# Optimization experiments

Hardware: AMD Instinct MI355X
Metric: run time of the kernel (lower is better)

Reference implementation:

```python
import jax, jax.numpy as jnp
import numpy as np
from math import sqrt

D_MODEL = 1024
N_HEADS = 16
FFN = 4096
B, N = 2, 2048
EPS = 1e-5


def _layernorm(x, g, b):
    mu = jnp.mean(x, -1, keepdims=True)
    var = jnp.mean((x - mu) ** 2, -1, keepdims=True)
    return (x - mu) * jax.lax.rsqrt(var + EPS) * g + b


def setup_inputs() -> dict:
    key = jax.random.key(0)
    ks = jax.random.split(key, 12)
    s = 1.0 / sqrt(D_MODEL)
    sf = 1.0 / sqrt(FFN)
    inp = {
        "tgt": jax.random.normal(ks[0], (B, N, D_MODEL), jnp.float32),
        # True = masked. Causal: query i may attend to keys j <= i.
        "tgt_mask": jnp.triu(jnp.ones((N, N), jnp.bool_), k=1),
        "tgt_key_pad_mask": jnp.zeros((B, N), jnp.bool_),
        "Wq": jax.random.uniform(ks[1], (D_MODEL, D_MODEL), jnp.float32, -s, s),
        "Wk": jax.random.uniform(ks[2], (D_MODEL, D_MODEL), jnp.float32, -s, s),
        "Wv": jax.random.uniform(ks[3], (D_MODEL, D_MODEL), jnp.float32, -s, s),
        "Wo": jax.random.uniform(ks[4], (D_MODEL, D_MODEL), jnp.float32, -s, s),
        "bo": jax.random.uniform(ks[5], (D_MODEL,), jnp.float32, -s, s),
        "W1": jax.random.uniform(ks[6], (FFN, D_MODEL), jnp.float32, -s, s),
        "b1": jax.random.uniform(ks[7], (FFN,), jnp.float32, -s, s),
        "W2": jax.random.uniform(ks[8], (D_MODEL, FFN), jnp.float32, -sf, sf),
        "b2": jax.random.uniform(ks[9], (D_MODEL,), jnp.float32, -sf, sf),
        "g1": jnp.ones((D_MODEL,), jnp.float32),
        "beta1": jnp.zeros((D_MODEL,), jnp.float32),
        "g2": jnp.ones((D_MODEL,), jnp.float32),
        "beta2": jnp.zeros((D_MODEL,), jnp.float32),
    }
    return inp


def _mha(x, tgt_mask, pad_mask, Wq, Wk, Wv, Wo, bo):
    b, n, d = x.shape
    dk = d // N_HEADS
    q = (x @ Wq.T).reshape(b, n, N_HEADS, dk).transpose(0, 2, 1, 3)  # bhnd
    k = (x @ Wk.T).reshape(b, n, N_HEADS, dk).transpose(0, 2, 1, 3)
    v = (x @ Wv.T).reshape(b, n, N_HEADS, dk).transpose(0, 2, 1, 3)
    scores = jnp.einsum("bhqd,bhkd->bhqk", q, k) / sqrt(dk)
    mask = tgt_mask[None, None, :, :] | pad_mask[:, None, None, :]
    scores = jnp.where(mask, -jnp.inf, scores)
    att = jax.nn.softmax(scores, axis=-1)
    out = jnp.einsum("bhqk,bhkd->bhqd", att, v).transpose(0, 2, 1, 3).reshape(b, n, d)
    return out @ Wo.T + bo


def reference(tgt, tgt_mask, tgt_key_pad_mask, Wq, Wk, Wv, Wo, bo,
              W1, b1, W2, b2, g1, beta1, g2, beta2):
    # PostNorm logic (pre_norm=False), dropout=0 (eval)
    h = _mha(tgt, tgt_mask, tgt_key_pad_mask, Wq, Wk, Wv, Wo, bo)
    x = _layernorm(tgt + h, g1, beta1)
    m = jax.nn.gelu(x @ W1.T + b1, approximate=True) @ W2.T + b2
    return _layernorm(x + m, g2, beta2)
```

## Files before the change

### kernel.cpp

```cpp
#include <hip/hip_runtime.h>


#define DEV __device__ __forceinline__

typedef __attribute__((ext_vector_type(4)))  float f32x4;
typedef __attribute__((ext_vector_type(16))) float f32x16;
typedef __attribute__((ext_vector_type(8)))  short s16x8;

static constexpr int Bb   = 2;
static constexpr int NN   = 2048;
static constexpr int DM   = 1024;
static constexpr int HH   = 16;
static constexpr int DK   = 64;
static constexpr int FF   = 4096;
static constexpr int ROWS = Bb * NN;

#define AS1(p) ((const __attribute__((address_space(1))) void*)(p))
#define AS3(p) ((__attribute__((address_space(3))) void*)(p))

DEV unsigned short f2bf(float f) {
  unsigned u = __float_as_uint(f);
  u += 0x7fff + ((u >> 16) & 1);
  return (unsigned short)(u >> 16);
}
DEV float fexp2(float x) {
  float r;
  asm("v_exp_f32 %0, %1" : "=v"(r) : "v"(x));
  return r;
}
DEV unsigned cvtpk(float lo, float hi) {
  unsigned r;
  asm("v_cvt_pk_bf16_f32 %0, %1, %2" : "=v"(r) : "v"(lo), "v"(hi));
  return r;
}

__global__ __launch_bounds__(256) void k_cast7(
    const float* __restrict__ tgt, const float* __restrict__ Wq,
    const float* __restrict__ Wk, const float* __restrict__ Wv,
    const float* __restrict__ Wo, const float* __restrict__ W1,
    const float* __restrict__ W2,
    ushort* __restrict__ xb, ushort* __restrict__ wqb,
    ushort* __restrict__ w1b, ushort* __restrict__ w2b) {
  const int i = blockIdx.x * 256 + threadIdx.x;
  constexpr int S0 = 1048576;
  constexpr int S1 = 262144;
  const float4* src;
  ushort* dstp;
  if (i < S0)               { src = (const float4*)tgt + i;            dstp = xb  + (size_t)i * 4; }
  else if (i < S0 + S1)     { src = (const float4*)Wq + (i - S0);      dstp = wqb + (size_t)(i - S0) * 4; }
  else if (i < S0 + 2 * S1) { src = (const float4*)Wk + (i - S0 - S1); dstp = wqb + (size_t)(i - S0) * 4; }
  else if (i < S0 + 3 * S1) { src = (const float4*)Wv + (i - S0 - 2 * S1); dstp = wqb + (size_t)(i - S0) * 4; }
  else if (i < S0 + 4 * S1) { src = (const float4*)Wo + (i - S0 - 3 * S1); dstp = wqb + (size_t)(i - S0) * 4; }
  else if (i < 3 * S0)      { src = (const float4*)W1 + (i - 2 * S0);  dstp = w1b + (size_t)(i - 2 * S0) * 4; }
  else                      { src = (const float4*)W2 + (i - 3 * S0);  dstp = w2b + (size_t)(i - 3 * S0) * 4; }
  float4 v = *src;
  ushort4 o;
  o.x = f2bf(v.x); o.y = f2bf(v.y); o.z = f2bf(v.z); o.w = f2bf(v.w);
  *reinterpret_cast<ushort4*>(dstp) = o;
}

template <int EPI, int BN, bool QKV, int SPLITK>
__global__ __launch_bounds__(256) void k_gemm(
    const ushort* __restrict__ A, const ushort* __restrict__ Bt,
    const float* __restrict__ bias, const float* __restrict__ resid,
    ushort* __restrict__ Cb, float* __restrict__ Cf,
    int K, int nbx) {
  __shared__ ushort As[3][128][32];
  __shared__ ushort Bs[3][BN][32];

  const int t = threadIdx.x;
  const int lane = t & 63, w = t >> 6;
  const int lr = lane & 15, lg = lane >> 4;
  const int lrow = lane >> 2, lc8 = (lane & 3) * 8;

  const int nwg = gridDim.x;
  const int bid = blockIdx.x;
  const int q8 = nwg >> 3, r8 = nwg & 7;
  const int xcd = bid & 7, lin = bid >> 3;
  int wg = (xcd < r8 ? xcd * (q8 + 1) : r8 * (q8 + 1) + (xcd - r8) * q8) + lin;
  int kc = 0;
  if constexpr (SPLITK == 2) { kc = wg & 1; wg >>= 1; }
  const int band = wg / (4 * nbx);
  const int inn  = wg % (4 * nbx);
  const int by = band * 4 + (inn & 3);
  const int bx = inn >> 2;

  const int bRow = by * 128;
  const int bCol = bx * BN;
  const int Kc = K / SPLITK;
  const int kofs = kc * Kc;
  const int nk = Kc / 32;

  constexpr int NW = BN / 32;
  const int wRow = (w >> 1) * 64, wCol = (w & 1) * (BN / 2);

  const f32x4 zero = {0.f, 0.f, 0.f, 0.f};
  f32x4 acc[4][NW];
#pragma unroll
  for (int m = 0; m < 4; ++m)
#pragma unroll
    for (int n = 0; n < NW; ++n) acc[m][n] = zero;

  auto stage = [&](int buf, int tile) {
    const int kb = kofs + tile * 32;
#pragma unroll
    for (int i = 0; i < 2; ++i) {
      int rr = w * 32 + i * 16;
      __builtin_amdgcn_global_load_lds(
          AS1(A + (size_t)(bRow + rr + lrow) * K + kb + lc8),
          AS3(&As[buf][rr][0]), 16, 0, 0);
    }
#pragma unroll
    for (int i = 0; i < BN / 64; ++i) {
      int rr = w * (BN / 4) + i * 16;
      __builtin_amdgcn_global_load_lds(
          AS1(Bt + (size_t)(bCol + rr + lrow) * K + kb + lc8),
          AS3(&Bs[buf][rr][0]), 16, 0, 0);
    }
  };

  stage(0, 0);
  stage(1, 1);
  for (int tt = 0; tt < nk; ++tt) {
    const int cur = tt % 3;
    if (tt + 2 < nk) {
      stage((tt + 2) % 3, tt + 2);
      if constexpr (BN == 128) asm volatile("s_waitcnt vmcnt(8)" ::: "memory");
      else                     asm volatile("s_waitcnt vmcnt(6)" ::: "memory");
    } else if (tt + 1 < nk) {
      if constexpr (BN == 128) asm volatile("s_waitcnt vmcnt(4)" ::: "memory");
      else                     asm volatile("s_waitcnt vmcnt(3)" ::: "memory");
    } else {
      asm volatile("s_waitcnt vmcnt(0)" ::: "memory");
    }
    __builtin_amdgcn_s_barrier();
    __builtin_amdgcn_sched_barrier(0);

    s16x8 af[4], bfr[NW];
#pragma unroll
    for (int m = 0; m < 4; ++m)
      af[m] = *reinterpret_cast<const s16x8*>(&As[cur][wRow + m * 16 + lr][lg * 8]);
#pragma unroll
    for (int n = 0; n < NW; ++n)
      bfr[n] = *reinterpret_cast<const s16x8*>(&Bs[cur][wCol + n * 16 + lr][lg * 8]);
#pragma unroll
    for (int m = 0; m < 4; ++m)
#pragma unroll
      for (int n = 0; n < NW; ++n)
        acc[m][n] = __builtin_amdgcn_mfma_f32_16x16x32_bf16(af[m], bfr[n], acc[m][n], 0, 0, 0);

    asm volatile("s_waitcnt lgkmcnt(0)" ::: "memory");
    __builtin_amdgcn_s_barrier();
    __builtin_amdgcn_sched_barrier(0);
  }

  ushort* CbOut = Cb;
  int colBase = bCol, Ncols = nbx * BN, third = 0;
  if (QKV) {
    third = bCol >> 10;
    CbOut = Cb + (size_t)third * ROWS * DM;
    colBase = bCol & 1023;
    Ncols = DM;
  }
#pragma unroll
  for (int m = 0; m < 4; ++m) {
    int gr = bRow + wRow + m * 16 + lg * 4;
#pragma unroll
    for (int n = 0; n < NW; ++n) {
      int gc = colBase + wCol + n * 16 + lr;
      float bv = (EPI == 1 || EPI == 2) ? bias[gc] : 0.0f;
#pragma unroll
      for (int r = 0; r < 4; ++r) {
        int nr = gr + r;
        float v = acc[m][n][r] + bv;
        if (EPI == 3) {
          Cf[((size_t)kc * ROWS + nr) * Ncols + gc] = v;
        } else if (EPI == 2) {
          size_t idx = (size_t)nr * Ncols + gc;
          Cf[idx] = v + resid[idx];
        } else if (EPI == 1) {
          size_t idx = (size_t)nr * Ncols + gc;
          float u = v + 0.044715f * v * v * v;
          float g = v / (1.0f + __expf(-1.5957691216057308f * u));
          CbOut[idx] = f2bf(g);
        } else {
          int gcs = gc;
          if (QKV && third == 1)
            gcs = (gc & ~63) | ((gc ^ ((nr & 7) << 3)) & 63);
          CbOut[(size_t)nr * Ncols + gcs] = f2bf(v);
        }
      }
    }
  }
}

__global__ __launch_bounds__(256) void k_vt(const ushort* __restrict__ V,
                                            ushort* __restrict__ vT) {
  __shared__ ushort Ls[64][72];
  const int t = threadIdx.x;
  const int n0 = blockIdx.x * 64;
  const int bh = blockIdx.y;
  const int b = bh >> 4, h = bh & 15;
  const int n = t >> 2;
#pragma unroll
  for (int half = 0; half < 2; ++half) {
    int c8 = ((t & 3) + half * 4) * 8;
    int4 v = *reinterpret_cast<const int4*>(
        V + ((size_t)(b * NN + n0 + n)) * DM + h * DK + c8);
    *reinterpret_cast<int4*>(&Ls[n][c8]) = v;
  }
  __syncthreads();
  const int d = t >> 2;
#pragma unroll
  for (int half = 0; half < 2; ++half) {
    int c = (t & 3) + half * 4;
    ushort tmp[8];
#pragma unroll
    for (int j = 0; j < 8; ++j) tmp[j] = Ls[c * 8 + j][d];
    size_t out = ((size_t)bh * DK + d) * NN + n0 + ((c ^ (d & 7)) * 8);
    *reinterpret_cast<int4*>(vT + out) = *reinterpret_cast<const int4*>(tmp);
  }
}

template <int WB, int RED>
__global__ __launch_bounds__(256) void k_ln(const float* __restrict__ in,
                                            const float* __restrict__ p0,
                                            const float* __restrict__ p1,
                                            const float* __restrict__ pb,
                                            const float* __restrict__ g,
                                            const float* __restrict__ bta,
                                            float* __restrict__ outf,
                                            ushort* __restrict__ outb) {
  const int row = blockIdx.x;
  const int t = threadIdx.x;
  float4 v = reinterpret_cast<const float4*>(in + (size_t)row * DM)[t];
  if (RED) {
    float4 a = reinterpret_cast<const float4*>(p0 + (size_t)row * DM)[t];
    float4 b = reinterpret_cast<const float4*>(p1 + (size_t)row * DM)[t];
    float4 c = reinterpret_cast<const float4*>(pb)[t];
    v.x += a.x + b.x + c.x;
    v.y += a.y + b.y + c.y;
    v.z += a.z + b.z + c.z;
    v.w += a.w + b.w + c.w;
  }
  float s1 = v.x + v.y + v.z + v.w;
  float s2 = v.x * v.x + v.y * v.y + v.z * v.z + v.w * v.w;
#pragma unroll
  for (int m = 32; m; m >>= 1) {
    s1 += __shfl_xor(s1, m, 64);
    s2 += __shfl_xor(s2, m, 64);
  }
  __shared__ float red[2][4];
  if ((t & 63) == 0) { red[0][t >> 6] = s1; red[1][t >> 6] = s2; }
  __syncthreads();
  s1 = red[0][0] + red[0][1] + red[0][2] + red[0][3];
  s2 = red[1][0] + red[1][1] + red[1][2] + red[1][3];
  const float mu = s1 * (1.0f / DM);
  const float var = s2 * (1.0f / DM) - mu * mu;
  const float rstd = rsqrtf(var + 1e-5f);
  float4 gv = reinterpret_cast<const float4*>(g)[t];
  float4 bv = reinterpret_cast<const float4*>(bta)[t];
  float4 o;
  o.x = (v.x - mu) * rstd * gv.x + bv.x;
  o.y = (v.y - mu) * rstd * gv.y + bv.y;
  o.z = (v.z - mu) * rstd * gv.z + bv.z;
  o.w = (v.w - mu) * rstd * gv.w + bv.w;
  reinterpret_cast<float4*>(outf + (size_t)row * DM)[t] = o;
  if (WB) {
    ushort4 ob;
    ob.x = f2bf(o.x); ob.y = f2bf(o.y); ob.z = f2bf(o.z); ob.w = f2bf(o.w);
    reinterpret_cast<ushort4*>(outb + (size_t)row * DM)[t] = ob;
  }
}

static __device__ const unsigned char SCHED40[40][2] = {
  {15,0},{15,1},{15,2},{15,3}, {14,0},{14,1},{14,2},{14,3},
  {13,0},{13,1},{13,2},{13,3}, {12,0},{12,1},{12,2},{12,3},
  {11,0},{11,1},{11,2}, {10,0},{10,1},{10,2},
  {9,0},{9,1},{9,2}, {8,0},{8,1},{8,2},
  {7,0},{7,1}, {6,0},{6,1}, {5,0},{5,1}, {4,0},{4,1},
  {3,0},{2,0},{1,0},{0,0}};

__global__ __launch_bounds__(256) void k_attn(const ushort* __restrict__ Q,
                                              const ushort* __restrict__ Kb,
                                              const ushort* __restrict__ vT,
                                              ushort* __restrict__ O,
                                              float* __restrict__ Op,
                                              float* __restrict__ ml) {
  __shared__ ushort Ks[2][64 * 64];
  __shared__ ushort Vs[2][64 * 64];

  const int t = threadIdx.x;
  const int bid = blockIdx.x;
  const int xcd = bid & 7, j = bid >> 3;
  const int head = j & 3, e = j >> 2;
  const int qi = SCHED40[e][0], seg = SCHED40[e][1];
  const int bh = xcd * 4 + head;
  const int ntiles = 2 * qi + 2;
  const int nseg = (2 * qi + 9) >> 3;
  const int tb = ntiles / nseg, rem = ntiles % nseg;
  const int kt0 = seg * tb + (seg < rem ? seg : rem);
  const int kt1 = kt0 + tb + (seg < rem ? 1 : 0);

  const int lane = t & 63, wid = t >> 6;
  const int l31 = lane & 31, hi = lane >> 5;
  const int q0w = qi * 128 + wid * 32;
  const size_t qbase = ((size_t)(bh >> 4) * NN) * DM + (bh & 15) * DK;
  const size_t vbase = (size_t)bh * DK * NN;

  const float C = 0.18033688011112043f;

  s16x8 qf[4];
#pragma unroll
  for (int c = 0; c < 4; ++c)
    qf[c] = *reinterpret_cast<const s16x8*>(Q + qbase + (size_t)(q0w + l31) * DM + c * 16 + hi * 8);

  float mrun = -1e30f, lrun = 0.f, negcm = 1e30f;
  f32x16 accO[2];
#pragma unroll
  for (int dt = 0; dt < 2; ++dt)
#pragma unroll
    for (int r = 0; r < 16; ++r) accO[dt][r] = 0.f;

  auto stage = [&](int buf, int kt) {
    const int kk = kt * 64;
#pragma unroll
    for (int i = 0; i < 2; ++i) {
      int row0 = wid * 16 + i * 8;
      __builtin_amdgcn_global_load_lds(
          AS1(Kb + qbase + (size_t)(kk + row0 + (lane >> 3)) * DM + (lane & 7) * 8),
          AS3(&Ks[buf][row0 * 64]), 16, 0, 0);
      __builtin_amdgcn_global_load_lds(
          AS1(vT + vbase + (size_t)(row0 + (lane >> 3)) * NN + kk + (lane & 7) * 8),
          AS3(&Vs[buf][row0 * 64]), 16, 0, 0);
    }
  };

  stage(0, kt0);
  for (int kt = kt0, li = 0; kt < kt1; ++kt, ++li) {
    const int cur = li & 1;
    const int kk = kt * 64;
    __syncthreads();
    if (kt + 1 < kt1) stage(cur ^ 1, kt + 1);

    if (kk <= q0w + 31) {
      const char* KsB = (const char*)Ks[cur];
      const char* VsB = (const char*)Vs[cur];
      const bool diag = (kk + 64 > q0w);
      const int nsub = (kk + 32 <= q0w + 31) ? 2 : 1;

      f32x16 st[2];
      __builtin_amdgcn_s_setprio(1);
#pragma unroll
      for (int sub = 0; sub < 2; ++sub) {
        if (sub >= nsub) break;
#pragma unroll
        for (int r = 0; r < 16; ++r) st[sub][r] = 0.f;
        const int row = sub * 32 + l31;
        const int swz = (row & 7) << 4;
#pragma unroll
        for (int c = 0; c < 4; ++c) {
          s16x8 kf = *reinterpret_cast<const s16x8*>(KsB + row * 128 + ((c * 32 + hi * 16) ^ swz));
          st[sub] = __builtin_amdgcn_mfma_f32_32x32x16_bf16(kf, qf[c], st[sub], 0, 0, 0);
        }
      }
      __builtin_amdgcn_s_setprio(0);

      const int q = q0w + l31;
      float p[32];
#pragma unroll
      for (int sub = 0; sub < 2; ++sub) {
        if (sub >= nsub) break;
#pragma unroll
        for (int r = 0; r < 16; ++r) {
          float v = st[sub][r];
          if (diag) {
            int kl = sub * 32 + (r & 3) + 8 * (r >> 2) + 4 * hi;
            if (kk + kl > q) v = -1e30f;
          }
          p[sub * 16 + r] = v;
        }
      }
      float a[16];
#pragma unroll
      for (int i = 0; i < 16; ++i) a[i] = (nsub == 2) ? fmaxf(p[i], p[i + 16]) : p[i];
#pragma unroll
      for (int s = 8; s; s >>= 1)
#pragma unroll
        for (int i = 0; i < 8; ++i) if (i < s) a[i] = fmaxf(a[i], a[i + s]);
      float rm = fmaxf(a[0], __shfl_xor(a[0], 32, 64));

      if (__any(rm > mrun)) {
        const float mn = fmaxf(mrun, rm);
        const float alpha = fexp2(C * (mrun - mn));
        mrun = mn;
        negcm = -C * mn;
        lrun *= alpha;
#pragma unroll
        for (int dt = 0; dt < 2; ++dt) accO[dt] *= alpha;
      }

#pragma unroll
      for (int sub = 0; sub < 2; ++sub) {
        if (sub >= nsub) break;
#pragma unroll
        for (int i = 0; i < 16; ++i)
          p[sub * 16 + i] = fexp2(fmaf(p[sub * 16 + i], C, negcm));
      }
#pragma unroll
      for (int i = 0; i < 16; ++i) a[i] = (nsub == 2) ? (p[i] + p[i + 16]) : p[i];
#pragma unroll
      for (int s = 8; s; s >>= 1)
#pragma unroll
        for (int i = 0; i < 8; ++i) if (i < s) a[i] += a[i + s];
      lrun += a[0] + __shfl_xor(a[0], 32, 64);

      s16x8 pf[4];
#pragma unroll
      for (int sub = 0; sub < 2; ++sub) {
        if (sub >= nsub) break;
#pragma unroll
        for (int hf = 0; hf < 2; ++hf) {
          const float* pp = &p[sub * 16 + hf * 8];
          unsigned X0 = cvtpk(pp[0], pp[1]);
          unsigned X1 = cvtpk(pp[2], pp[3]);
          unsigned Y0 = cvtpk(pp[4], pp[5]);
          unsigned Y1 = cvtpk(pp[6], pp[7]);
          asm volatile("v_permlane32_swap_b32 %0, %1" : "+v"(X0), "+v"(Y0));
          asm volatile("v_permlane32_swap_b32 %0, %1" : "+v"(X1), "+v"(Y1));
          union { unsigned u[4]; s16x8 v; } uu;
          uu.u[0] = X0; uu.u[1] = X1; uu.u[2] = Y0; uu.u[3] = Y1;
          pf[sub * 2 + hf] = uu.v;
        }
      }

      __builtin_amdgcn_s_setprio(1);
#pragma unroll
      for (int dt = 0; dt < 2; ++dt) {
        const int d = dt * 32 + l31;
        const int vswz = (d & 7) << 4;
#pragma unroll
        for (int kc = 0; kc < 4; ++kc) {
          if (kc >= nsub * 2) break;
          s16x8 vf = *reinterpret_cast<const s16x8*>(VsB + d * 128 + ((kc * 32 + hi * 16) ^ vswz));
          accO[dt] = __builtin_amdgcn_mfma_f32_32x32x16_bf16(vf, pf[kc], accO[dt], 0, 0, 0);
        }
      }
      __builtin_amdgcn_s_setprio(0);
    }
  }

  if (nseg == 1) {
    const int q = q0w + l31;
    const float inv = 1.0f / lrun;
#pragma unroll
    for (int dt = 0; dt < 2; ++dt)
#pragma unroll
      for (int rg = 0; rg < 4; ++rg) {
        int d0 = 8 * rg + 4 * hi + 32 * dt;
        ushort4 ov;
        ov.x = f2bf(accO[dt][rg * 4 + 0] * inv);
        ov.y = f2bf(accO[dt][rg * 4 + 1] * inv);
        ov.z = f2bf(accO[dt][rg * 4 + 2] * inv);
        ov.w = f2bf(accO[dt][rg * 4 + 3] * inv);
        *reinterpret_cast<ushort4*>(O + qbase + (size_t)q * DM + d0) = ov;
      }
  } else {
    const int pidx = (bh * 12 + (qi - 4)) * 4 + seg;
    float* op = Op + (size_t)pidx * (128 * 64);
    const int row = wid * 32 + l31;
#pragma unroll
    for (int dt = 0; dt < 2; ++dt)
#pragma unroll
      for (int rg = 0; rg < 4; ++rg) {
        int d0 = 8 * rg + 4 * hi + 32 * dt;
        f32x4 v4 = { accO[dt][rg * 4 + 0], accO[dt][rg * 4 + 1],
                     accO[dt][rg * 4 + 2], accO[dt][rg * 4 + 3] };
        *reinterpret_cast<f32x4*>(op + (size_t)row * 64 + d0) = v4;
      }
    if (hi == 0) {
      ml[(size_t)pidx * 256 + row * 2 + 0] = mrun;
      ml[(size_t)pidx * 256 + row * 2 + 1] = lrun;
    }
  }
}

__global__ __launch_bounds__(256) void k_amerge(const float* __restrict__ Op,
                                                const float* __restrict__ ml,
                                                ushort* __restrict__ O) {
  const int bid = blockIdx.x;
  const int bh = bid / 12, qq = bid % 12;
  const int qi = qq + 4;
  const int nseg = (2 * qi + 9) >> 3;
  const int t = threadIdx.x;
  const int row = t >> 1, dh = (t & 1) * 32;
  const float C = 0.18033688011112043f;
  const int pbase = (bh * 12 + qq) * 4;

  float M = -1e30f;
  for (int s = 0; s < nseg; ++s)
    M = fmaxf(M, ml[(size_t)(pbase + s) * 256 + row * 2 + 0]);
  float wsum = 0.f;
  for (int s = 0; s < nseg; ++s) {
    float ms = ml[(size_t)(pbase + s) * 256 + row * 2 + 0];
    float ls = ml[(size_t)(pbase + s) * 256 + row * 2 + 1];
    wsum += ls * fexp2(C * (ms - M));
  }
  const float inv = 1.0f / wsum;

  f32x4 acc[8];
#pragma unroll
  for (int i = 0; i < 8; ++i) acc[i] = (f32x4){0.f, 0.f, 0.f, 0.f};
  for (int s = 0; s < nseg; ++s) {
    float ws = fexp2(C * (ml[(size_t)(pbase + s) * 256 + row * 2 + 0] - M));
    const float* os = Op + (size_t)(pbase + s) * (128 * 64) + (size_t)row * 64 + dh;
#pragma unroll
    for (int i = 0; i < 8; ++i) {
      f32x4 v = reinterpret_cast<const f32x4*>(os)[i];
      acc[i] += v * ws;
    }
  }

  const int b = bh >> 4, h = bh & 15;
  const int n = qi * 128 + row;
  ushort* dst = O + ((size_t)(b * NN + n)) * DM + h * DK + dh;
#pragma unroll
  for (int i = 0; i < 8; ++i) {
    ushort4 ov;
    ov.x = f2bf(acc[i][0] * inv);
    ov.y = f2bf(acc[i][1] * inv);
    ov.z = f2bf(acc[i][2] * inv);
    ov.w = f2bf(acc[i][3] * inv);
    reinterpret_cast<ushort4*>(dst)[i] = ov;
  }
}

extern "C" void kernel_launch(void* const* d_in, const int* in_sizes, int n_in,
                              void* d_out, int out_size, void* d_ws, size_t ws_size,
                              hipStream_t stream) {
  const float* tgt = (const float*)d_in[0];
  const float* Wq  = (const float*)d_in[3];
  const float* Wk  = (const float*)d_in[4];
  const float* Wv  = (const float*)d_in[5];
  const float* Wo  = (const float*)d_in[6];
  const float* bo  = (const float*)d_in[7];
  const float* W1  = (const float*)d_in[8];
  const float* b1  = (const float*)d_in[9];
  const float* W2  = (const float*)d_in[10];
  const float* b2  = (const float*)d_in[11];
  const float* g1  = (const float*)d_in[12];
  const float* be1 = (const float*)d_in[13];
  const float* g2  = (const float*)d_in[14];
  const float* be2 = (const float*)d_in[15];

  char* ws = (char*)d_ws;
  size_t off = 0;
  auto alloc = [&](size_t bytes) {
    void* p = ws + off;
    off += (bytes + 255) & ~(size_t)255;
    return p;
  };
  ushort* xb   = (ushort*)alloc((size_t)ROWS * DM * 2);
  ushort* wqb  = (ushort*)alloc((size_t)DM * DM * 2);
  ushort* wkb  = (ushort*)alloc((size_t)DM * DM * 2);
  ushort* wvb  = (ushort*)alloc((size_t)DM * DM * 2);
  ushort* wob  = (ushort*)alloc((size_t)DM * DM * 2);
  ushort* w1b  = (ushort*)alloc((size_t)FF * DM * 2);
  ushort* w2b  = (ushort*)alloc((size_t)DM * FF * 2);
  ushort* qbuf = (ushort*)alloc((size_t)ROWS * DM * 2);
  ushort* kbuf = (ushort*)alloc((size_t)ROWS * DM * 2);
  ushort* vbuf = (ushort*)alloc((size_t)ROWS * DM * 2);
  ushort* vtb  = (ushort*)alloc((size_t)ROWS * DM * 2);
  ushort* atnb = (ushort*)alloc((size_t)ROWS * DM * 2);
  float*  h1   = (float*)alloc((size_t)ROWS * DM * 4);
  float*  x1f  = (float*)alloc((size_t)ROWS * DM * 4);
  ushort* x1b  = (ushort*)alloc((size_t)ROWS * DM * 2);
  ushort* t1b  = (ushort*)alloc((size_t)ROWS * FF * 2);
  float*  mlb  = (float*)alloc((size_t)1536 * 256 * 4);
  float*  Opb  = h1;
  float*  pp   = (float*)qbuf;
  (void)ws_size; (void)in_sizes; (void)n_in; (void)out_size;
  (void)wkb; (void)wvb; (void)kbuf;

  dim3 blk(256);
  k_cast7<<<dim3(16384), blk, 0, stream>>>(tgt, Wq, Wk, Wv, Wo, W1, W2,
                                           xb, wqb, w1b, w2b);

  k_gemm<0, 128, true, 1><<<dim3(24 * 32), blk, 0, stream>>>(
      xb, wqb, nullptr, nullptr, qbuf, nullptr, DM, 24);

  k_vt<<<dim3(NN / 64, Bb * HH), blk, 0, stream>>>(vbuf, vtb);

  k_attn<<<dim3(1280), blk, 0, stream>>>(qbuf, kbuf, vtb, atnb, Opb, mlb);
  k_amerge<<<dim3(384), blk, 0, stream>>>(Opb, mlb, atnb);

  k_gemm<2, 64, false, 1><<<dim3(16 * 32), blk, 0, stream>>>(
      atnb, wob, bo, tgt, nullptr, h1, DM, 16);
  k_ln<1, 0><<<dim3(ROWS), blk, 0, stream>>>(h1, nullptr, nullptr, nullptr,
                                             g1, be1, x1f, x1b);

  k_gemm<1, 128, false, 1><<<dim3(32 * 32), blk, 0, stream>>>(
      x1b, w1b, b1, nullptr, t1b, nullptr, DM, 32);
  k_gemm<3, 64, false, 2><<<dim3(2 * 16 * 32), blk, 0, stream>>>(
      t1b, w2b, nullptr, nullptr, nullptr, pp, FF, 16);
  k_ln<0, 1><<<dim3(ROWS), blk, 0, stream>>>(x1f, pp, pp + (size_t)ROWS * DM, b2,
                                             g2, be2, (float*)d_out, nullptr);
}
```

Before: 269.3 us.

## Store GEMM LDS tiles in MFMA fragment order and use 8x8 tile swizzle

The GEMM's global-to-LDS loads now write each 16-row by 32-column chunk in the exact per-lane order that the MFMA fragment read expects. Each lane can then fetch its operand with a contiguous 16-byte LDS read at a lane-linear address, which is meant to remove LDS bank conflicts from the previous row-major 64-byte-stride reads. Workgroup-to-tile mapping also changes from 4-row bands to 8x8 super-tiles for better L2 reuse. The new mapping assumes nbx is divisible by 8 and the grid is a multiple of 64; other shapes would mis-map.

```diff
diff --git a/kernel.cpp b/kernel.cpp
--- a/kernel.cpp
+++ b/kernel.cpp
@@ -71,7 +71,6 @@
   const int t = threadIdx.x;
   const int lane = t & 63, w = t >> 6;
   const int lr = lane & 15, lg = lane >> 4;
-  const int lrow = lane >> 2, lc8 = (lane & 3) * 8;
 
   const int nwg = gridDim.x;
   const int bid = blockIdx.x;
@@ -80,10 +79,10 @@
   int wg = (xcd < r8 ? xcd * (q8 + 1) : r8 * (q8 + 1) + (xcd - r8) * q8) + lin;
   int kc = 0;
   if constexpr (SPLITK == 2) { kc = wg & 1; wg >>= 1; }
-  const int band = wg / (4 * nbx);
-  const int inn  = wg % (4 * nbx);
-  const int by = band * 4 + (inn & 3);
-  const int bx = inn >> 2;
+  const int sC = nbx >> 3;
+  const int st = wg >> 6, wi = wg & 63;
+  const int by = (st / sC) * 8 + (wi >> 3);
+  const int bx = (st % sC) * 8 + (wi & 7);
 
   const int bRow = by * 128;
   const int bCol = bx * BN;
@@ -92,7 +91,6 @@
   const int nk = Kc / 32;
 
   constexpr int NW = BN / 32;
-  const int wRow = (w >> 1) * 64, wCol = (w & 1) * (BN / 2);
 
   const f32x4 zero = {0.f, 0.f, 0.f, 0.f};
   f32x4 acc[4][NW];
@@ -101,21 +99,37 @@
 #pragma unroll
     for (int n = 0; n < NW; ++n) acc[m][n] = zero;
 
+  char* AsB = (char*)As;
+  char* BsB = (char*)Bs;
+  constexpr int ABUF = 8192;
+  constexpr int BBUF = BN * 64;
+
   auto stage = [&](int buf, int tile) {
     const int kb = kofs + tile * 32;
+    const int aC = lg * 8;
 #pragma unroll
     for (int i = 0; i < 2; ++i) {
-      int rr = w * 32 + i * 16;
+      int c = w * 2 + i;
+      int row = (c >> 2) * 64 + (c & 3) * 16 + lr;
       __builtin_amdgcn_global_load_lds(
-          AS1(A + (size_t)(bRow + rr + lrow) * K + kb + lc8),
-          AS3(&As[buf][rr][0]), 16, 0, 0);
-    }
-#pragma unroll
-    for (int i = 0; i < BN / 64; ++i) {
-      int rr = w * (BN / 4) + i * 16;
+          AS1(A + (size_t)(bRow + row) * K + kb + aC),
+          AS3(AsB + buf * ABUF + c * 1024), 16, 0, 0);
+    }
+    if constexpr (BN == 128) {
+#pragma unroll
+      for (int i = 0; i < 2; ++i) {
+        int c = w * 2 + i;
+        int row = (c >> 2) * 64 + (c & 3) * 16 + lr;
+        __builtin_amdgcn_global_load_lds(
+            AS1(Bt + (size_t)(bCol + row) * K + kb + aC),
+            AS3(BsB + buf * BBUF + c * 1024), 16, 0, 0);
+      }
+    } else {
+      int c = w;
+      int row = (c >> 1) * 32 + (c & 1) * 16 + lr;
       __builtin_amdgcn_global_load_lds(
-          AS1(Bt + (size_t)(bCol + rr + lrow) * K + kb + lc8),
-          AS3(&Bs[buf][rr][0]), 16, 0, 0);
+          AS1(Bt + (size_t)(bCol + row) * K + kb + aC),
+          AS3(BsB + buf * BBUF + c * 1024), 16, 0, 0);
     }
   };
 
@@ -136,13 +150,15 @@
     __builtin_amdgcn_s_barrier();
     __builtin_amdgcn_sched_barrier(0);
 
+    const char* Ab = AsB + cur * ABUF + (w >> 1) * 4096 + lane * 16;
+    const char* Bb = BsB + cur * BBUF + (w & 1) * (BBUF / 2) + lane * 16;
     s16x8 af[4], bfr[NW];
 #pragma unroll
     for (int m = 0; m < 4; ++m)
-      af[m] = *reinterpret_cast<const s16x8*>(&As[cur][wRow + m * 16 + lr][lg * 8]);
+      af[m] = *reinterpret_cast<const s16x8*>(Ab + m * 1024);
 #pragma unroll
     for (int n = 0; n < NW; ++n)
-      bfr[n] = *reinterpret_cast<const s16x8*>(&Bs[cur][wCol + n * 16 + lr][lg * 8]);
+      bfr[n] = *reinterpret_cast<const s16x8*>(Bb + n * 1024);
 #pragma unroll
     for (int m = 0; m < 4; ++m)
 #pragma unroll
@@ -154,6 +170,7 @@
     __builtin_amdgcn_sched_barrier(0);
   }
 
+  const int wRow = (w >> 1) * 64, wCol = (w & 1) * (BN / 2);
   ushort* CbOut = Cb;
   int colBase = bCol, Ncols = nbx * BN, third = 0;
   if (QKV) {
@@ -512,12 +529,12 @@
 #pragma unroll
   for (int i = 0; i < 8; ++i) acc[i] = (f32x4){0.f, 0.f, 0.f, 0.f};
   for (int s = 0; s < nseg; ++s) {
-    float ws = fexp2(C * (ml[(size_t)(pbase + s) * 256 + row * 2 + 0] - M));
+    float wsc = fexp2(C * (ml[(size_t)(pbase + s) * 256 + row * 2 + 0] - M));
     const float* os = Op + (size_t)(pbase + s) * (128 * 64) + (size_t)row * 64 + dh;
 #pragma unroll
     for (int i = 0; i < 8; ++i) {
       f32x4 v = reinterpret_cast<const f32x4*>(os)[i];
-      acc[i] += v * ws;
+      acc[i] += v * wsc;
     }
   }
 
```

Measured after the change: 362.5 us. 34.6% more time.

## Fuse V transpose into QKV GEMM epilogue and use double-buffered GEMM staging

Applied to the files above, without the earlier changes.

The QKV GEMM epilogue now writes the V third straight into the swizzled per-head transposed layout that attention expects, so the separate k_vt transpose kernel and its extra V read/write pass are removed. It also shrinks the GEMM LDS pipeline from three stages to two, with matching vmcnt waits. That cuts shared memory per block and may raise occupancy, but leaves less load latency hidden. The fused V stores are 8-byte scattered writes strided by sequence length, which coalesce worse than the old transposed stores. The V output location relies on vtb sitting right after vbuf in the workspace.

```diff
diff --git a/kernel.cpp b/kernel.cpp
--- a/kernel.cpp
+++ b/kernel.cpp
@@ -65,8 +65,8 @@
     const float* __restrict__ bias, const float* __restrict__ resid,
     ushort* __restrict__ Cb, float* __restrict__ Cf,
     int K, int nbx) {
-  __shared__ ushort As[3][128][32];
-  __shared__ ushort Bs[3][BN][32];
+  __shared__ ushort As[2][128][32];
+  __shared__ ushort Bs[2][BN][32];
 
   const int t = threadIdx.x;
   const int lane = t & 63, w = t >> 6;
@@ -120,14 +120,10 @@
   };
 
   stage(0, 0);
-  stage(1, 1);
   for (int tt = 0; tt < nk; ++tt) {
-    const int cur = tt % 3;
-    if (tt + 2 < nk) {
-      stage((tt + 2) % 3, tt + 2);
-      if constexpr (BN == 128) asm volatile("s_waitcnt vmcnt(8)" ::: "memory");
-      else                     asm volatile("s_waitcnt vmcnt(6)" ::: "memory");
-    } else if (tt + 1 < nk) {
+    const int cur = tt & 1;
+    if (tt + 1 < nk) {
+      stage(cur ^ 1, tt + 1);
       if constexpr (BN == 128) asm volatile("s_waitcnt vmcnt(4)" ::: "memory");
       else                     asm volatile("s_waitcnt vmcnt(3)" ::: "memory");
     } else {
@@ -168,6 +164,20 @@
 #pragma unroll
     for (int n = 0; n < NW; ++n) {
       int gc = colBase + wCol + n * 16 + lr;
+      if (QKV && third == 2) {
+        int h = gc >> 6, d = gc & 63;
+        int b = gr >> 11, ntok = gr & (NN - 1);
+        size_t basev = ((size_t)(b * HH + h) * DK + d) * NN;
+        int nb = ntok & ~63, c = (ntok >> 3) & 7, j0 = ntok & 7;
+        ushort4 ov;
+        ov.x = f2bf(acc[m][n][0]);
+        ov.y = f2bf(acc[m][n][1]);
+        ov.z = f2bf(acc[m][n][2]);
+        ov.w = f2bf(acc[m][n][3]);
+        ushort* VT = Cb + (size_t)3 * ROWS * DM;
+        *reinterpret_cast<ushort4*>(VT + basev + nb + ((c ^ (d & 7)) << 3) + j0) = ov;
+        continue;
+      }
       float bv = (EPI == 1 || EPI == 2) ? bias[gc] : 0.0f;
 #pragma unroll
       for (int r = 0; r < 4; ++r) {
@@ -191,34 +201,6 @@
         }
       }
     }
-  }
-}
-
-__global__ __launch_bounds__(256) void k_vt(const ushort* __restrict__ V,
-                                            ushort* __restrict__ vT) {
-  __shared__ ushort Ls[64][72];
-  const int t = threadIdx.x;
-  const int n0 = blockIdx.x * 64;
-  const int bh = blockIdx.y;
-  const int b = bh >> 4, h = bh & 15;
-  const int n = t >> 2;
-#pragma unroll
-  for (int half = 0; half < 2; ++half) {
-    int c8 = ((t & 3) + half * 4) * 8;
-    int4 v = *reinterpret_cast<const int4*>(
-        V + ((size_t)(b * NN + n0 + n)) * DM + h * DK + c8);
-    *reinterpret_cast<int4*>(&Ls[n][c8]) = v;
-  }
-  __syncthreads();
-  const int d = t >> 2;
-#pragma unroll
-  for (int half = 0; half < 2; ++half) {
-    int c = (t & 3) + half * 4;
-    ushort tmp[8];
-#pragma unroll
-    for (int j = 0; j < 8; ++j) tmp[j] = Ls[c * 8 + j][d];
-    size_t out = ((size_t)bh * DK + d) * NN + n0 + ((c ^ (d & 7)) * 8);
-    *reinterpret_cast<int4*>(vT + out) = *reinterpret_cast<const int4*>(tmp);
   }
 }
 
@@ -512,12 +494,12 @@
 #pragma unroll
   for (int i = 0; i < 8; ++i) acc[i] = (f32x4){0.f, 0.f, 0.f, 0.f};
   for (int s = 0; s < nseg; ++s) {
-    float ws = fexp2(C * (ml[(size_t)(pbase + s) * 256 + row * 2 + 0] - M));
+    float wsc = fexp2(C * (ml[(size_t)(pbase + s) * 256 + row * 2 + 0] - M));
     const float* os = Op + (size_t)(pbase + s) * (128 * 64) + (size_t)row * 64 + dh;
 #pragma unroll
     for (int i = 0; i < 8; ++i) {
       f32x4 v = reinterpret_cast<const f32x4*>(os)[i];
-      acc[i] += v * ws;
+      acc[i] += v * wsc;
     }
   }
 
@@ -580,7 +562,7 @@
   float*  Opb  = h1;
   float*  pp   = (float*)qbuf;
   (void)ws_size; (void)in_sizes; (void)n_in; (void)out_size;
-  (void)wkb; (void)wvb; (void)kbuf;
+  (void)wkb; (void)wvb; (void)kbuf; (void)vbuf; (void)vtb;
 
   dim3 blk(256);
   k_cast7<<<dim3(16384), blk, 0, stream>>>(tgt, Wq, Wk, Wv, Wo, W1, W2,
@@ -588,8 +570,6 @@
 
   k_gemm<0, 128, true, 1><<<dim3(24 * 32), blk, 0, stream>>>(
       xb, wqb, nullptr, nullptr, qbuf, nullptr, DM, 24);
-
-  k_vt<<<dim3(NN / 64, Bb * HH), blk, 0, stream>>>(vbuf, vtb);
 
   k_attn<<<dim3(1280), blk, 0, stream>>>(qbuf, kbuf, vtb, atnb, Opb, mlb);
   k_amerge<<<dim3(384), blk, 0, stream>>>(Opb, mlb, atnb);
```

Result: faster. 263.3 us (-2.2%).
